# Optimization experiments

Measured on AMD Instinct MI355X. Metric: run time of the kernel, lower is better.

Reference implementation:

```python
import jax, jax.numpy as jnp
import numpy as np


def adder2d(x, w, stride=1, padding=0):
    """AdderNet conv: out = -sum_{ci,kh,kw} |x_patch - w|, supports groups.
    x: [B,Cin,H,W], w: [Cout, Cin//G, K, K]. Loops only over K*K kernel taps."""
    B, Cin, H, W = x.shape
    Cout, Cin_g, K, _ = w.shape
    G = Cin // Cin_g
    Co_g = Cout // G
    xp = jnp.pad(x, ((0, 0), (0, 0), (padding, padding), (padding, padding)))
    Ho = (H + 2 * padding - K) // stride + 1
    Wo = (W + 2 * padding - K) // stride + 1
    wg = w.reshape(G, Co_g, Cin_g, K, K)
    out = jnp.zeros((B, Cout, Ho, Wo), x.dtype)
    for kh in range(K):
        for kw in range(K):
            xs = jax.lax.slice(
                xp, (0, 0, kh, kw),
                (B, Cin, kh + stride * (Ho - 1) + 1, kw + stride * (Wo - 1) + 1),
                (1, 1, stride, stride))  # [B,Cin,Ho,Wo]
            xs = xs.reshape(B, G, 1, Cin_g, Ho, Wo)
            wt = wg[:, :, :, kh, kw][None, :, :, :, None, None]  # [1,G,Co_g,Cin_g,1,1]
            out = out - jnp.abs(xs - wt).sum(3).reshape(B, Cout, Ho, Wo)
    return out


def bn(x, g, b, m, v, eps=1e-5):
    inv = g / jnp.sqrt(v + eps)
    return x * inv[None, :, None, None] + (b - m * inv)[None, :, None, None]


def setup_inputs() -> dict:
    key = jax.random.key(0)
    ks = jax.random.split(key, 18)
    d = {}
    d["x"] = jax.random.normal(ks[0], (8, 256, 28, 28), jnp.float32)
    d["w1"] = jax.random.normal(ks[1], (64, 256, 1, 1), jnp.float32) * 0.05
    d["w_peg"] = jax.random.normal(ks[2], (64, 1, 3, 3), jnp.float32) * 0.05
    d["w2"] = jax.random.normal(ks[3], (64, 64, 3, 3), jnp.float32) * 0.05
    d["w3"] = jax.random.normal(ks[4], (256, 64, 1, 1), jnp.float32) * 0.05
    for i, (c, tag) in enumerate([(64, "1"), (64, "2"), (256, "3")]):
        d["g" + tag] = jax.random.uniform(ks[5 + 4 * i], (c,), jnp.float32, 0.5, 1.5)
        d["b" + tag] = jax.random.normal(ks[6 + 4 * i], (c,), jnp.float32) * 0.1
        d["m" + tag] = jax.random.normal(ks[7 + 4 * i], (c,), jnp.float32) * 0.1
        d["v" + tag] = jax.random.uniform(ks[8 + 4 * i], (c,), jnp.float32, 0.5, 1.5)
    return d


def reference(x, w1, w_peg, w2, w3, g1, b1, m1, v1, g2, b2, m2, v2, g3, b3, m3, v3):
    residual = x  # downsample is Identity (stride=1, inplanes==outplanes)
    h = adder2d(x, w1)                       # 1x1 adder conv 256->64
    h = adder2d(h, w_peg, stride=1, padding=1)  # PEG: depthwise 3x3 adder conv
    h = jax.nn.relu(bn(h, g1, b1, m1, v1))
    h = adder2d(h, w2, padding=1)            # 3x3 adder conv 64->64
    h = jax.nn.relu(bn(h, g2, b2, m2, v2))
    h = adder2d(h, w3)                       # 1x1 adder conv 64->256
    h = bn(h, g3, b3, m3, v3)
    return jax.nn.relu(h + residual)
```

## Files before the change

kernel.cpp:

```cpp
#include <hip/hip_runtime.h>
#include <math.h>

#define PR 30
#define PC 32

__device__ __forceinline__ void tap3(const float4 a, const float2 b,
                                     const float w0, const float w1, const float w2,
                                     float4& acc) {
    acc.x += fabsf(a.x - w0) + fabsf(a.y - w1) + fabsf(a.z - w2);
    acc.y += fabsf(a.y - w0) + fabsf(a.z - w1) + fabsf(a.w - w2);
    acc.z += fabsf(a.z - w0) + fabsf(a.w - w1) + fabsf(b.x - w2);
    acc.w += fabsf(a.w - w0) + fabsf(b.x - w1) + fabsf(b.y - w2);
}

__global__ __launch_bounds__(448) void k1_adder1x1(const float* __restrict__ x,
                                                   const float* __restrict__ w1,
                                                   float* __restrict__ h1p) {
    __shared__ __align__(16) float smem[7168];
    float*  ws  = smem;
    float4* pl4 = (float4*)smem;
    const int tid    = threadIdx.x;
    const int cog    = tid & 3;
    const int pxg    = (tid >> 2) % 7;
    const int cic    = tid / 28;
    const int n      = blockIdx.x / 28;
    const int y      = blockIdx.x % 28;
    const int px0    = y * 28 + pxg * 4;
    const int cobase = blockIdx.y * 16;

    for (int idx = tid; idx < 4096; idx += 448) {
        int co = idx >> 8, ci = idx & 255;
        ws[ci * 20 + co] = w1[(size_t)(cobase + co) * 256 + ci];
    }
    __syncthreads();

    float4 acc0 = {0,0,0,0}, acc1 = acc0, acc2 = acc0, acc3 = acc0;
    const float* xp = x + ((size_t)n * 256 + cic * 16) * 784 + px0;
    const float* wp = ws + (cic * 16) * 20 + cog * 4;
    #pragma unroll 8
    for (int i = 0; i < 16; ++i) {
        float4 u = *(const float4*)(xp + (size_t)i * 784);
        float4 w = *(const float4*)(wp + i * 20);
        acc0.x += fabsf(u.x - w.x); acc0.y += fabsf(u.y - w.x); acc0.z += fabsf(u.z - w.x); acc0.w += fabsf(u.w - w.x);
        acc1.x += fabsf(u.x - w.y); acc1.y += fabsf(u.y - w.y); acc1.z += fabsf(u.z - w.y); acc1.w += fabsf(u.w - w.y);
        acc2.x += fabsf(u.x - w.z); acc2.y += fabsf(u.y - w.z); acc2.z += fabsf(u.z - w.z); acc2.w += fabsf(u.w - w.z);
        acc3.x += fabsf(u.x - w.w); acc3.y += fabsf(u.y - w.w); acc3.z += fabsf(u.z - w.w); acc3.w += fabsf(u.w - w.w);
    }
    __syncthreads();
    const int pbase = pxg * 16 + cog * 4;
    pl4[cic * 112 + pbase + 0] = acc0;
    pl4[cic * 112 + pbase + 1] = acc1;
    pl4[cic * 112 + pbase + 2] = acc2;
    pl4[cic * 112 + pbase + 3] = acc3;
    __syncthreads();

    if (tid < 112) {
        const int rpxg = tid >> 4;
        const int rcog = (tid >> 2) & 3;
        const int j    = tid & 3;
        const int rb   = rpxg * 16 + rcog * 4 + j;
        float4 s = pl4[rb];
        #pragma unroll
        for (int c = 1; c < 16; ++c) {
            float4 t = pl4[c * 112 + rb];
            s.x += t.x; s.y += t.y; s.z += t.z; s.w += t.w;
        }
        const int co = cobase + rcog * 4 + j;
        float* op = h1p + ((size_t)(n * 64 + co) * PR + y + 1) * PC + rpxg * 4 + 1;
        op[0] = -s.x; op[1] = -s.y; op[2] = -s.z; op[3] = -s.w;
        if (rpxg == 0) op[-1] = 0.f;
        if (rpxg == 6) { op[4] = 0.f; op[5] = 0.f; op[6] = 0.f; }
    }
    if (y == 0 || y == 27) {
        const int prow = (y == 0) ? 0 : 29;
        for (int idx = tid; idx < 512; idx += 448) {
            int coi = idx >> 5, col = idx & 31;
            h1p[((size_t)(n * 64 + cobase + coi) * PR + prow) * PC + col] = 0.f;
        }
    }
}

__global__ __launch_bounds__(256) void k2_peg_bn_relu(const float* __restrict__ h1p,
                                                      const float* __restrict__ wp,
                                                      const float* __restrict__ w2,
                                                      const float* __restrict__ w3,
                                                      const float* __restrict__ g1,
                                                      const float* __restrict__ b1,
                                                      const float* __restrict__ m1,
                                                      const float* __restrict__ v1,
                                                      float* __restrict__ h2p,
                                                      float* __restrict__ w2t,
                                                      float* __restrict__ w3t) {
    const int t = blockIdx.x * 256 + threadIdx.x;
    if (t < 100352) {
        const int pxq = t % 196;
        const int c   = (t / 196) & 63;
        const int n   = t / (196 * 64);
        const int p0  = pxq * 4;
        const int y   = p0 / 28, xx = p0 % 28;
        const float* base = h1p + ((size_t)(n * 64 + c) * PR + y) * PC + xx;
        const float* wc   = wp + c * 9;
        float4 acc = {0,0,0,0};
        #pragma unroll
        for (int kh = 0; kh < 3; ++kh) {
            float4 a = *(const float4*)(base + kh * PC);
            float2 b = *(const float2*)(base + kh * PC + 4);
            tap3(a, b, wc[kh * 3 + 0], wc[kh * 3 + 1], wc[kh * 3 + 2], acc);
        }
        float inv = g1[c] * rsqrtf(v1[c] + 1e-5f);
        float bb  = b1[c] - m1[c] * inv;
        float* op = h2p + ((size_t)(n * 64 + c) * PR + y + 1) * PC + xx + 1;
        op[0] = fmaxf(-acc.x * inv + bb, 0.f);
        op[1] = fmaxf(-acc.y * inv + bb, 0.f);
        op[2] = fmaxf(-acc.z * inv + bb, 0.f);
        op[3] = fmaxf(-acc.w * inv + bb, 0.f);
    } else if (t < 190464) {
        int i = t - 100352;
        int plane = i / 176, r = i % 176;
        int row, col;
        if (r < 64) { row = (r >> 5) * 29; col = r & 31; }
        else { int j = r - 64; row = 1 + (j >> 2); int k = j & 3; col = k ? 28 + k : 0; }
        h2p[(size_t)plane * (PR * PC) + row * PC + col] = 0.f;
    } else if (t < 227328) {
        int i = t - 190464;
        int r = i >> 6, c2 = i & 63;
        w2t[i] = w2[(size_t)c2 * 576 + r];
    } else if (t < 243712) {
        int i = t - 227328;
        int ci = i >> 8, c2 = i & 255;
        w3t[i] = w3[(size_t)c2 * 64 + ci];
    }
}

__global__ __launch_bounds__(512) void k3_part(const float* __restrict__ h2p,
                                               const float* __restrict__ w2t,
                                               float* __restrict__ h3part) {
    __shared__ __align__(16) float h2t[1728];
    __shared__ __align__(16) float wt[4896];
    const int tid  = threadIdx.x;
    const int lane = tid & 63;
    const int oct  = __builtin_amdgcn_readfirstlane(tid >> 6);
    const int col  = lane & 31;
    const int cih  = lane >> 5;
    const int Y0   = blockIdx.x * 4;
    const int ciQ  = blockIdx.y;
    const int n    = blockIdx.z;

    for (int i = tid; i < 384; i += 512) {
        int ci = i / 48, rem = i % 48;
        int r = rem >> 3, c4 = rem & 7;
        *(float4*)(h2t + ci * 216 + r * 36 + c4 * 4) =
            *(const float4*)(h2p + ((size_t)(n * 64 + ciQ * 8 + ci) * PR + Y0 + r) * PC + c4 * 4);
    }
    for (int i = tid; i < 1152; i += 512) {
        int row = i >> 4, c4 = i & 15;
        *(float4*)(wt + row * 68 + c4 * 4) =
            *(const float4*)(w2t + ((size_t)ciQ * 72 + row) * 64 + c4 * 4);
    }
    __syncthreads();

    float acc[4][8];
    #pragma unroll
    for (int r = 0; r < 4; ++r)
        #pragma unroll
        for (int j = 0; j < 8; ++j) acc[r][j] = 0.f;

    #pragma unroll
    for (int i = 0; i < 4; ++i) {
        const int ci_l = cih * 4 + i;
        float win[6][3];
        #pragma unroll
        for (int r = 0; r < 6; ++r)
            #pragma unroll
            for (int kw = 0; kw < 3; ++kw)
                win[r][kw] = h2t[ci_l * 216 + r * 36 + col + kw];
        const float* wrow = wt + ci_l * 612 + oct * 8;
        #pragma unroll
        for (int kh = 0; kh < 3; ++kh) {
            #pragma unroll
            for (int kw = 0; kw < 3; ++kw) {
                float4 wa = *(const float4*)(wrow + (kh * 3 + kw) * 68);
                float4 wb = *(const float4*)(wrow + (kh * 3 + kw) * 68 + 4);
                #pragma unroll
                for (int r = 0; r < 4; ++r) {
                    const float xv = win[r + kh][kw];
                    acc[r][0] += fabsf(xv - wa.x); acc[r][1] += fabsf(xv - wa.y);
                    acc[r][2] += fabsf(xv - wa.z); acc[r][3] += fabsf(xv - wa.w);
                    acc[r][4] += fabsf(xv - wb.x); acc[r][5] += fabsf(xv - wb.y);
                    acc[r][6] += fabsf(xv - wb.z); acc[r][7] += fabsf(xv - wb.w);
                }
            }
        }
    }
    #pragma unroll
    for (int r = 0; r < 4; ++r)
        #pragma unroll
        for (int j = 0; j < 8; ++j)
            acc[r][j] += __shfl_xor(acc[r][j], 32, 64);

    if (cih == 0 && col < 28) {
        #pragma unroll
        for (int r = 0; r < 4; ++r)
            #pragma unroll
            for (int j = 0; j < 8; ++j)
                h3part[(((size_t)ciQ * 8 + n) * 64 + oct * 8 + j) * 784 + (Y0 + r) * 28 + col] = acc[r][j];
    }
}

__global__ __launch_bounds__(512) void k6_fused(const float* __restrict__ h3part,
                                                const float* __restrict__ w3t,
                                                const float* __restrict__ x,
                                                const float* __restrict__ g2,
                                                const float* __restrict__ b2,
                                                const float* __restrict__ m2,
                                                const float* __restrict__ v2,
                                                const float* __restrict__ g3,
                                                const float* __restrict__ b3,
                                                const float* __restrict__ m3,
                                                const float* __restrict__ v3,
                                                float* __restrict__ out) {
    __shared__ __align__(16) float h3t[2048];
    __shared__ __align__(16) float w3s[16896];
    const int tid = threadIdx.x;
    const int Y   = blockIdx.x;
    const int n   = blockIdx.y;

    if (tid < 448) {
        const int co = tid / 7, c4 = tid % 7;
        size_t base = ((size_t)n * 64 + co) * 784 + Y * 28 + c4 * 4;
        const size_t qstride = (size_t)8 * 64 * 784;
        float4 s = *(const float4*)(h3part + base);
        #pragma unroll
        for (int qq = 1; qq < 8; ++qq) {
            float4 t = *(const float4*)(h3part + qq * qstride + base);
            s.x += t.x; s.y += t.y; s.z += t.z; s.w += t.w;
        }
        float inv = g2[co] * rsqrtf(v2[co] + 1e-5f);
        float bb  = b2[co] - m2[co] * inv;
        float4 o;
        o.x = fmaxf(-s.x * inv + bb, 0.f);
        o.y = fmaxf(-s.y * inv + bb, 0.f);
        o.z = fmaxf(-s.z * inv + bb, 0.f);
        o.w = fmaxf(-s.w * inv + bb, 0.f);
        *(float4*)(h3t + co * 32 + c4 * 4) = o;
    }
    for (int iq = tid; iq < 4096; iq += 512) {
        int ci = iq >> 6, cq = iq & 63;
        *(float4*)(w3s + ci * 264 + cq * 4) =
            *(const float4*)(w3t + (size_t)ci * 256 + cq * 4);
    }
    __syncthreads();

    {
        const int bl = tid & 63;
        const int pg = tid >> 6;
        float4 c0 = {0,0,0,0}, c1 = c0, c2 = c0, c3 = c0;
        const float* hb = h3t + pg * 4;
        const float* wb = w3s + bl * 4;
        #pragma unroll 8
        for (int ci = 0; ci < 64; ++ci) {
            float4 h = *(const float4*)(hb + ci * 32);
            float4 w = *(const float4*)(wb + ci * 264);
            c0.x += fabsf(h.x - w.x); c0.y += fabsf(h.y - w.x); c0.z += fabsf(h.z - w.x); c0.w += fabsf(h.w - w.x);
            c1.x += fabsf(h.x - w.y); c1.y += fabsf(h.y - w.y); c1.z += fabsf(h.z - w.y); c1.w += fabsf(h.w - w.y);
            c2.x += fabsf(h.x - w.z); c2.y += fabsf(h.y - w.z); c2.z += fabsf(h.z - w.z); c2.w += fabsf(h.w - w.z);
            c3.x += fabsf(h.x - w.w); c3.y += fabsf(h.y - w.w); c3.z += fabsf(h.z - w.w); c3.w += fabsf(h.w - w.w);
        }
        if (pg < 7) {
            float4 accs[4] = {c0, c1, c2, c3};
            #pragma unroll
            for (int j = 0; j < 4; ++j) {
                const int co = bl * 4 + j;
                float inv = g3[co] * rsqrtf(v3[co] + 1e-5f);
                float bb  = b3[co] - m3[co] * inv;
                size_t obase = ((size_t)n * 256 + co) * 784 + Y * 28 + pg * 4;
                float4 r = *(const float4*)(x + obase);
                float4 o;
                o.x = fmaxf(-accs[j].x * inv + bb + r.x, 0.f);
                o.y = fmaxf(-accs[j].y * inv + bb + r.y, 0.f);
                o.z = fmaxf(-accs[j].z * inv + bb + r.z, 0.f);
                o.w = fmaxf(-accs[j].w * inv + bb + r.w, 0.f);
                *(float4*)(out + obase) = o;
            }
        }
    }
}

extern "C" void kernel_launch(void* const* d_in, const int* in_sizes, int n_in,
                              void* d_out, int out_size, void* d_ws, size_t ws_size,
                              hipStream_t stream) {
    const float* x  = (const float*)d_in[0];
    const float* w1 = (const float*)d_in[1];
    const float* wp = (const float*)d_in[2];
    const float* w2 = (const float*)d_in[3];
    const float* w3 = (const float*)d_in[4];
    const float* g1 = (const float*)d_in[5];
    const float* b1 = (const float*)d_in[6];
    const float* m1 = (const float*)d_in[7];
    const float* v1 = (const float*)d_in[8];
    const float* g2 = (const float*)d_in[9];
    const float* b2 = (const float*)d_in[10];
    const float* m2 = (const float*)d_in[11];
    const float* v2 = (const float*)d_in[12];
    const float* g3 = (const float*)d_in[13];
    const float* b3 = (const float*)d_in[14];
    const float* m3 = (const float*)d_in[15];
    const float* v3 = (const float*)d_in[16];
    float* out = (float*)d_out;

    float* wsf     = (float*)d_ws;
    float* h1p     = wsf;
    float* h2p     = wsf + 491520;
    float* w2t     = wsf + 983040;
    float* w3t     = wsf + 1019904;
    float* h3part  = wsf + 1036288;

    k1_adder1x1<<<dim3(224, 4), 448, 0, stream>>>(x, w1, h1p);
    k2_peg_bn_relu<<<dim3(952), 256, 0, stream>>>(h1p, wp, w2, w3,
                                                  g1, b1, m1, v1, h2p, w2t, w3t);
    k3_part<<<dim3(7, 8, 8), 512, 0, stream>>>(h2p, w2t, h3part);
    k6_fused<<<dim3(28, 8), 512, 0, stream>>>(h3part, w3t, x,
                                              g2, b2, m2, v2, g3, b3, m3, v3, out);
}
```

Before: 59.14 us.

## Enlarge k3 row tile to 7 and split k6 over output-channel halves

k3_part now computes 7 output rows per block instead of 4. This reuses each loaded weight across more rows and halves the grid (4x8x8 blocks), at the cost of more accumulator registers and a partial unroll of the ci loop. k6_fused now splits the 256 output channels across two blocks of 256 threads and reads w3t straight from global memory rather than staging it in LDS. That cuts shared memory per block and doubles the block count, but each block repeats the h3part reduction.

```diff
diff --git a/kernel.cpp b/kernel.cpp
--- a/kernel.cpp
+++ b/kernel.cpp
@@ -135,21 +135,21 @@
 __global__ __launch_bounds__(512) void k3_part(const float* __restrict__ h2p,
                                                const float* __restrict__ w2t,
                                                float* __restrict__ h3part) {
-    __shared__ __align__(16) float h2t[1728];
+    __shared__ __align__(16) float h2t[2592];
     __shared__ __align__(16) float wt[4896];
     const int tid  = threadIdx.x;
     const int lane = tid & 63;
     const int oct  = __builtin_amdgcn_readfirstlane(tid >> 6);
     const int col  = lane & 31;
     const int cih  = lane >> 5;
-    const int Y0   = blockIdx.x * 4;
+    const int Y0   = blockIdx.x * 7;
     const int ciQ  = blockIdx.y;
     const int n    = blockIdx.z;
 
-    for (int i = tid; i < 384; i += 512) {
-        int ci = i / 48, rem = i % 48;
+    for (int i = tid; i < 576; i += 512) {
+        int ci = i / 72, rem = i % 72;
         int r = rem >> 3, c4 = rem & 7;
-        *(float4*)(h2t + ci * 216 + r * 36 + c4 * 4) =
+        *(float4*)(h2t + ci * 324 + r * 36 + c4 * 4) =
             *(const float4*)(h2p + ((size_t)(n * 64 + ciQ * 8 + ci) * PR + Y0 + r) * PC + c4 * 4);
     }
     for (int i = tid; i < 1152; i += 512) {
@@ -159,21 +159,21 @@
     }
     __syncthreads();
 
-    float acc[4][8];
+    float acc[7][8];
     #pragma unroll
-    for (int r = 0; r < 4; ++r)
+    for (int r = 0; r < 7; ++r)
         #pragma unroll
         for (int j = 0; j < 8; ++j) acc[r][j] = 0.f;
 
-    #pragma unroll
+    #pragma unroll 2
     for (int i = 0; i < 4; ++i) {
         const int ci_l = cih * 4 + i;
-        float win[6][3];
-        #pragma unroll
-        for (int r = 0; r < 6; ++r)
+        float win[9][3];
+        #pragma unroll
+        for (int r = 0; r < 9; ++r)
             #pragma unroll
             for (int kw = 0; kw < 3; ++kw)
-                win[r][kw] = h2t[ci_l * 216 + r * 36 + col + kw];
+                win[r][kw] = h2t[ci_l * 324 + r * 36 + col + kw];
         const float* wrow = wt + ci_l * 612 + oct * 8;
         #pragma unroll
         for (int kh = 0; kh < 3; ++kh) {
@@ -182,7 +182,7 @@
                 float4 wa = *(const float4*)(wrow + (kh * 3 + kw) * 68);
                 float4 wb = *(const float4*)(wrow + (kh * 3 + kw) * 68 + 4);
                 #pragma unroll
-                for (int r = 0; r < 4; ++r) {
+                for (int r = 0; r < 7; ++r) {
                     const float xv = win[r + kh][kw];
                     acc[r][0] += fabsf(xv - wa.x); acc[r][1] += fabsf(xv - wa.y);
                     acc[r][2] += fabsf(xv - wa.z); acc[r][3] += fabsf(xv - wa.w);
@@ -193,21 +193,21 @@
         }
     }
     #pragma unroll
-    for (int r = 0; r < 4; ++r)
+    for (int r = 0; r < 7; ++r)
         #pragma unroll
         for (int j = 0; j < 8; ++j)
             acc[r][j] += __shfl_xor(acc[r][j], 32, 64);
 
     if (cih == 0 && col < 28) {
         #pragma unroll
-        for (int r = 0; r < 4; ++r)
+        for (int r = 0; r < 7; ++r)
             #pragma unroll
             for (int j = 0; j < 8; ++j)
                 h3part[(((size_t)ciQ * 8 + n) * 64 + oct * 8 + j) * 784 + (Y0 + r) * 28 + col] = acc[r][j];
     }
 }
 
-__global__ __launch_bounds__(512) void k6_fused(const float* __restrict__ h3part,
+__global__ __launch_bounds__(256) void k6_fused(const float* __restrict__ h3part,
                                                 const float* __restrict__ w3t,
                                                 const float* __restrict__ x,
                                                 const float* __restrict__ g2,
@@ -220,14 +220,14 @@
                                                 const float* __restrict__ v3,
                                                 float* __restrict__ out) {
     __shared__ __align__(16) float h3t[2048];
-    __shared__ __align__(16) float w3s[16896];
     const int tid = threadIdx.x;
     const int Y   = blockIdx.x;
-    const int n   = blockIdx.y;
-
-    if (tid < 448) {
-        const int co = tid / 7, c4 = tid % 7;
-        size_t base = ((size_t)n * 64 + co) * 784 + Y * 28 + c4 * 4;
+    const int coH = blockIdx.y;
+    const int n   = blockIdx.z;
+
+    for (int iq = tid; iq < 448; iq += 256) {
+        const int ci = iq / 7, c4 = iq % 7;
+        size_t base = ((size_t)n * 64 + ci) * 784 + Y * 28 + c4 * 4;
         const size_t qstride = (size_t)8 * 64 * 784;
         float4 s = *(const float4*)(h3part + base);
         #pragma unroll
@@ -235,32 +235,28 @@
             float4 t = *(const float4*)(h3part + qq * qstride + base);
             s.x += t.x; s.y += t.y; s.z += t.z; s.w += t.w;
         }
-        float inv = g2[co] * rsqrtf(v2[co] + 1e-5f);
-        float bb  = b2[co] - m2[co] * inv;
+        float inv = g2[ci] * rsqrtf(v2[ci] + 1e-5f);
+        float bb  = b2[ci] - m2[ci] * inv;
         float4 o;
         o.x = fmaxf(-s.x * inv + bb, 0.f);
         o.y = fmaxf(-s.y * inv + bb, 0.f);
         o.z = fmaxf(-s.z * inv + bb, 0.f);
         o.w = fmaxf(-s.w * inv + bb, 0.f);
-        *(float4*)(h3t + co * 32 + c4 * 4) = o;
-    }
-    for (int iq = tid; iq < 4096; iq += 512) {
-        int ci = iq >> 6, cq = iq & 63;
-        *(float4*)(w3s + ci * 264 + cq * 4) =
-            *(const float4*)(w3t + (size_t)ci * 256 + cq * 4);
+        *(float4*)(h3t + ci * 32 + c4 * 4) = o;
     }
     __syncthreads();
 
     {
-        const int bl = tid & 63;
-        const int pg = tid >> 6;
+        const int bl = tid & 31;
+        const int pg = tid >> 5;
+        const int co0 = coH * 128 + bl * 4;
         float4 c0 = {0,0,0,0}, c1 = c0, c2 = c0, c3 = c0;
         const float* hb = h3t + pg * 4;
-        const float* wb = w3s + bl * 4;
+        const float* wb = w3t + co0;
         #pragma unroll 8
         for (int ci = 0; ci < 64; ++ci) {
             float4 h = *(const float4*)(hb + ci * 32);
-            float4 w = *(const float4*)(wb + ci * 264);
+            float4 w = *(const float4*)(wb + (size_t)ci * 256);
             c0.x += fabsf(h.x - w.x); c0.y += fabsf(h.y - w.x); c0.z += fabsf(h.z - w.x); c0.w += fabsf(h.w - w.x);
             c1.x += fabsf(h.x - w.y); c1.y += fabsf(h.y - w.y); c1.z += fabsf(h.z - w.y); c1.w += fabsf(h.w - w.y);
             c2.x += fabsf(h.x - w.z); c2.y += fabsf(h.y - w.z); c2.z += fabsf(h.z - w.z); c2.w += fabsf(h.w - w.z);
@@ -270,7 +266,7 @@
             float4 accs[4] = {c0, c1, c2, c3};
             #pragma unroll
             for (int j = 0; j < 4; ++j) {
-                const int co = bl * 4 + j;
+                const int co = co0 + j;
                 float inv = g3[co] * rsqrtf(v3[co] + 1e-5f);
                 float bb  = b3[co] - m3[co] * inv;
                 size_t obase = ((size_t)n * 256 + co) * 784 + Y * 28 + pg * 4;
@@ -318,7 +314,7 @@
     k1_adder1x1<<<dim3(224, 4), 448, 0, stream>>>(x, w1, h1p);
     k2_peg_bn_relu<<<dim3(952), 256, 0, stream>>>(h1p, wp, w2, w3,
                                                   g1, b1, m1, v1, h2p, w2t, w3t);
-    k3_part<<<dim3(7, 8, 8), 512, 0, stream>>>(h2p, w2t, h3part);
-    k6_fused<<<dim3(28, 8), 512, 0, stream>>>(h3part, w3t, x,
-                                              g2, b2, m2, v2, g3, b3, m3, v3, out);
-}
+    k3_part<<<dim3(4, 8, 8), 512, 0, stream>>>(h2p, w2t, h3part);
+    k6_fused<<<dim3(28, 2, 8), 256, 0, stream>>>(h3part, w3t, x,
+                                                 g2, b2, m2, v2, g3, b3, m3, v3, out);
+}
```

New measurement: 80.44 us. 36.0% more time.

## Fuse PEG depthwise conv and BN1 into k3 tile load, move weight transposes into k1

Applied to the files above, without the earlier changes.

Removes the separate k2 kernel. The w2/w3 transposes now run in otherwise idle threads of k1. k3 loads the padded h1 rows with a one-row halo into shared memory and computes the depthwise 3x3 adder conv, BN1 and ReLU itself, writing the h2 tile (with zero padding) directly into LDS. This eliminates one launch and the h2p global write and read round trip. In exchange, neighbouring k3 blocks recompute halo rows and k3 gains shared memory and a prologue stage.

```diff
diff --git a/kernel.cpp b/kernel.cpp
--- a/kernel.cpp
+++ b/kernel.cpp
@@ -15,7 +15,11 @@
 
 __global__ __launch_bounds__(448) void k1_adder1x1(const float* __restrict__ x,
                                                    const float* __restrict__ w1,
-                                                   float* __restrict__ h1p) {
+                                                   const float* __restrict__ w2,
+                                                   const float* __restrict__ w3,
+                                                   float* __restrict__ h1p,
+                                                   float* __restrict__ w2t,
+                                                   float* __restrict__ w3t) {
     __shared__ __align__(16) float smem[7168];
     float*  ws  = smem;
     float4* pl4 = (float4*)smem;
@@ -28,6 +32,19 @@
     const int px0    = y * 28 + pxg * 4;
     const int cobase = blockIdx.y * 16;
 
+    {
+        const int bid3 = blockIdx.x + 224 * blockIdx.y;
+        const int tg = bid3 * 448 + tid;
+        if (tg < 36864) {
+            int r = tg >> 6, c2 = tg & 63;
+            w2t[tg] = w2[(size_t)c2 * 576 + r];
+        } else if (tg < 53248) {
+            int i = tg - 36864;
+            int ci = i >> 8, c2 = i & 255;
+            w3t[i] = w3[(size_t)c2 * 64 + ci];
+        }
+    }
+
     for (int idx = tid; idx < 4096; idx += 448) {
         int co = idx >> 8, ci = idx & 255;
         ws[ci * 20 + co] = w1[(size_t)(cobase + co) * 256 + ci];
@@ -80,63 +97,18 @@
     }
 }
 
-__global__ __launch_bounds__(256) void k2_peg_bn_relu(const float* __restrict__ h1p,
-                                                      const float* __restrict__ wp,
-                                                      const float* __restrict__ w2,
-                                                      const float* __restrict__ w3,
-                                                      const float* __restrict__ g1,
-                                                      const float* __restrict__ b1,
-                                                      const float* __restrict__ m1,
-                                                      const float* __restrict__ v1,
-                                                      float* __restrict__ h2p,
-                                                      float* __restrict__ w2t,
-                                                      float* __restrict__ w3t) {
-    const int t = blockIdx.x * 256 + threadIdx.x;
-    if (t < 100352) {
-        const int pxq = t % 196;
-        const int c   = (t / 196) & 63;
-        const int n   = t / (196 * 64);
-        const int p0  = pxq * 4;
-        const int y   = p0 / 28, xx = p0 % 28;
-        const float* base = h1p + ((size_t)(n * 64 + c) * PR + y) * PC + xx;
-        const float* wc   = wp + c * 9;
-        float4 acc = {0,0,0,0};
-        #pragma unroll
-        for (int kh = 0; kh < 3; ++kh) {
-            float4 a = *(const float4*)(base + kh * PC);
-            float2 b = *(const float2*)(base + kh * PC + 4);
-            tap3(a, b, wc[kh * 3 + 0], wc[kh * 3 + 1], wc[kh * 3 + 2], acc);
-        }
-        float inv = g1[c] * rsqrtf(v1[c] + 1e-5f);
-        float bb  = b1[c] - m1[c] * inv;
-        float* op = h2p + ((size_t)(n * 64 + c) * PR + y + 1) * PC + xx + 1;
-        op[0] = fmaxf(-acc.x * inv + bb, 0.f);
-        op[1] = fmaxf(-acc.y * inv + bb, 0.f);
-        op[2] = fmaxf(-acc.z * inv + bb, 0.f);
-        op[3] = fmaxf(-acc.w * inv + bb, 0.f);
-    } else if (t < 190464) {
-        int i = t - 100352;
-        int plane = i / 176, r = i % 176;
-        int row, col;
-        if (r < 64) { row = (r >> 5) * 29; col = r & 31; }
-        else { int j = r - 64; row = 1 + (j >> 2); int k = j & 3; col = k ? 28 + k : 0; }
-        h2p[(size_t)plane * (PR * PC) + row * PC + col] = 0.f;
-    } else if (t < 227328) {
-        int i = t - 190464;
-        int r = i >> 6, c2 = i & 63;
-        w2t[i] = w2[(size_t)c2 * 576 + r];
-    } else if (t < 243712) {
-        int i = t - 227328;
-        int ci = i >> 8, c2 = i & 255;
-        w3t[i] = w3[(size_t)c2 * 64 + ci];
-    }
-}
-
-__global__ __launch_bounds__(512) void k3_part(const float* __restrict__ h2p,
+__global__ __launch_bounds__(512) void k3_part(const float* __restrict__ h1p,
+                                               const float* __restrict__ wpeg,
                                                const float* __restrict__ w2t,
+                                               const float* __restrict__ g1,
+                                               const float* __restrict__ b1,
+                                               const float* __restrict__ m1,
+                                               const float* __restrict__ v1,
                                                float* __restrict__ h3part) {
+    __shared__ __align__(16) float h1t[2304];
     __shared__ __align__(16) float h2t[1728];
     __shared__ __align__(16) float wt[4896];
+    __shared__ float wpg[72];
     const int tid  = threadIdx.x;
     const int lane = tid & 63;
     const int oct  = __builtin_amdgcn_readfirstlane(tid >> 6);
@@ -146,16 +118,41 @@
     const int ciQ  = blockIdx.y;
     const int n    = blockIdx.z;
 
-    for (int i = tid; i < 384; i += 512) {
-        int ci = i / 48, rem = i % 48;
-        int r = rem >> 3, c4 = rem & 7;
-        *(float4*)(h2t + ci * 216 + r * 36 + c4 * 4) =
-            *(const float4*)(h2p + ((size_t)(n * 64 + ciQ * 8 + ci) * PR + Y0 + r) * PC + c4 * 4);
+    {
+        int ci = tid >> 6, lr = (tid >> 3) & 7, c4 = tid & 7;
+        int gr = Y0 - 1 + lr;
+        gr = gr < 0 ? 0 : (gr > 29 ? 29 : gr);
+        *(float4*)(h1t + ci * 288 + lr * 36 + c4 * 4) =
+            *(const float4*)(h1p + ((size_t)(n * 64 + ciQ * 8 + ci) * PR + gr) * PC + c4 * 4);
     }
     for (int i = tid; i < 1152; i += 512) {
         int row = i >> 4, c4 = i & 15;
         *(float4*)(wt + row * 68 + c4 * 4) =
             *(const float4*)(w2t + ((size_t)ciQ * 72 + row) * 64 + c4 * 4);
+    }
+    if (tid < 72) wpg[tid] = wpeg[(ciQ * 8 + tid / 9) * 9 + tid % 9];
+    __syncthreads();
+
+    for (int i = tid; i < 1536; i += 512) {
+        int ci = i / 192, rem = i % 192;
+        int r = rem >> 5, c = rem & 31;
+        int pr = Y0 + r;
+        float val = 0.f;
+        if (c >= 1 && c <= 28 && pr >= 1 && pr <= 28) {
+            const float* hb = h1t + ci * 288 + r * 36 + (c - 1);
+            const float* wc = wpg + ci * 9;
+            float a = 0.f;
+            #pragma unroll
+            for (int kh = 0; kh < 3; ++kh)
+                #pragma unroll
+                for (int kw = 0; kw < 3; ++kw)
+                    a += fabsf(hb[kh * 36 + kw] - wc[kh * 3 + kw]);
+            const int gci = ciQ * 8 + ci;
+            float inv = g1[gci] * rsqrtf(v1[gci] + 1e-5f);
+            float bb  = b1[gci] - m1[gci] * inv;
+            val = fmaxf(-a * inv + bb, 0.f);
+        }
+        h2t[ci * 216 + r * 36 + c] = val;
     }
     __syncthreads();
 
@@ -310,15 +307,12 @@
 
     float* wsf     = (float*)d_ws;
     float* h1p     = wsf;
-    float* h2p     = wsf + 491520;
-    float* w2t     = wsf + 983040;
-    float* w3t     = wsf + 1019904;
-    float* h3part  = wsf + 1036288;
-
-    k1_adder1x1<<<dim3(224, 4), 448, 0, stream>>>(x, w1, h1p);
-    k2_peg_bn_relu<<<dim3(952), 256, 0, stream>>>(h1p, wp, w2, w3,
-                                                  g1, b1, m1, v1, h2p, w2t, w3t);
-    k3_part<<<dim3(7, 8, 8), 512, 0, stream>>>(h2p, w2t, h3part);
+    float* w2t     = wsf + 491520;
+    float* w3t     = wsf + 528384;
+    float* h3part  = wsf + 544768;
+
+    k1_adder1x1<<<dim3(224, 4), 448, 0, stream>>>(x, w1, w2, w3, h1p, w2t, w3t);
+    k3_part<<<dim3(7, 8, 8), 512, 0, stream>>>(h1p, wp, w2t, g1, b1, m1, v1, h3part);
     k6_fused<<<dim3(28, 8), 512, 0, stream>>>(h3part, w3t, x,
                                               g2, b2, m2, v2, g3, b3, m3, v3, out);
 }
```

Result: faster. 57.57 us, median of 2 (-2.7%).
